# Kernel tuning notes

Hardware: AMD Instinct MI355X
Metric: run time of the kernel (lower is better)

Reference implementation:

```python
import jax, jax.numpy as jnp
import numpy as np

D = 1024
H = 16
B = 4
S = 2048
NEG = -1000000000.0


def setup_inputs() -> dict:
    key = jax.random.key(0)
    ks = jax.random.split(key, 12)
    s = 0.02
    inp = {
        "Q": jax.random.normal(ks[0], (B, S, D), jnp.float32),
        "K": jax.random.normal(ks[1], (B, S, D), jnp.float32),
        "V": jax.random.normal(ks[2], (B, S, D), jnp.float32),
        # causal mask, broadcastable to [B, H, S, S]
        "mask": jnp.broadcast_to(jnp.tril(jnp.ones((S, S), bool)), (B, 1, S, S)),
        "Wq": jax.random.normal(ks[3], (D, D), jnp.float32) * s,
        "bq": jnp.zeros((D,), jnp.float32),
        "Wk": jax.random.normal(ks[4], (D, D), jnp.float32) * s,
        "bk": jnp.zeros((D,), jnp.float32),
        "Wv": jax.random.normal(ks[5], (D, D), jnp.float32) * s,
        "bv": jnp.zeros((D,), jnp.float32),
        "Wo": jax.random.normal(ks[6], (D, D), jnp.float32) * s,
        "bo": jnp.zeros((D,), jnp.float32),
    }
    return inp


def reference(Q, K, V, mask, Wq, bq, Wk, bk, Wv, bv, Wo, bo):
    d = D // H  # head dim
    def split(x):  # [B,S,D] -> [B,H,S,d]
        Bx, Sx, _ = x.shape
        return x.reshape(Bx, Sx, H, d).transpose(0, 2, 1, 3)

    q = split(Q @ Wq + bq)
    k = split(K @ Wk + bk)
    v = split(V @ Wv + bv)

    scores = jnp.einsum("bhsd,bhtd->bhst", q, k) / jnp.sqrt(jnp.float32(d))
    scores = jnp.where(mask, scores, NEG)
    attn = jax.nn.softmax(scores, axis=-1)
    out = jnp.einsum("bhst,bhtd->bhsd", attn, v)  # [B,H,S,d]
    out = out.transpose(0, 2, 1, 3).reshape(Q.shape[0], Q.shape[1], D)
    return out @ Wo + bo
```

## Files before the change

kernel.cpp:

```cpp
#include <hip/hip_runtime.h>
#include <hip/hip_bf16.h>
#include <type_traits>

#define DEV __device__ __forceinline__

typedef short bf16x8 __attribute__((ext_vector_type(8)));
typedef float f32x4 __attribute__((ext_vector_type(4)));
typedef float f32x16 __attribute__((ext_vector_type(16)));
typedef unsigned u32x4 __attribute__((ext_vector_type(4)));

static DEV unsigned short f2bf(float f) {
  unsigned u = __builtin_bit_cast(unsigned, f);
  u += 0x7FFFu + ((u >> 16) & 1u);
  return (unsigned short)(u >> 16);
}

static DEV unsigned cvtpk(float lo, float hi) {
  unsigned d;
  asm("v_cvt_pk_bf16_f32 %0, %1, %2" : "=v"(d) : "v"(lo), "v"(hi));
  return d;
}

static DEV void pl32(unsigned& x, unsigned& y) {
  asm("v_permlane32_swap_b32 %0, %1" : "+v"(x), "+v"(y));
}

static DEV float vmax3(float a, float b, float c) {
  float d;
  asm("v_max3_f32 %0, %1, %2, %3" : "=v"(d) : "v"(a), "v"(b), "v"(c));
  return d;
}

static DEV void gl_lds16(const unsigned short* g, unsigned short* l) {
  __builtin_amdgcn_global_load_lds(
      (const __attribute__((address_space(1))) unsigned*)g,
      (__attribute__((address_space(3))) unsigned*)l, 16, 0, 0);
}

#define QSCALE 0.18033688f

__global__ __launch_bounds__(256) void wtrans4(const float* __restrict__ W0,
                                               const float* __restrict__ W1,
                                               const float* __restrict__ W2,
                                               const float* __restrict__ W3,
                                               unsigned short* __restrict__ T0,
                                               unsigned short* __restrict__ T1,
                                               unsigned short* __restrict__ T2,
                                               unsigned short* __restrict__ T3) {
  const int z = blockIdx.z;
  const float* W = z == 0 ? W0 : z == 1 ? W1 : z == 2 ? W2 : W3;
  unsigned short* Wt = z == 0 ? T0 : z == 1 ? T1 : z == 2 ? T2 : T3;
  const float wsc = (z == 0) ? QSCALE : 1.0f;
  __shared__ __align__(16) unsigned short T[64][72];
  const int tid = threadIdx.x;
  const int k0 = blockIdx.x * 64, n0 = blockIdx.y * 64;
  const int r = tid >> 4, c4 = (tid & 15) * 4;
  for (int j = 0; j < 4; ++j) {
    int row = j * 16 + r;
    float4 v = *(const float4*)&W[(size_t)(k0 + row) * 1024 + n0 + c4];
    ushort4 w;
    w.x = f2bf(v.x * wsc); w.y = f2bf(v.y * wsc);
    w.z = f2bf(v.z * wsc); w.w = f2bf(v.w * wsc);
    *(ushort4*)&T[row][c4] = w;
  }
  __syncthreads();
  for (int j = 0; j < 4; ++j) {
    int n = j * 16 + r;
    ushort4 w;
    w.x = T[c4 + 0][n]; w.y = T[c4 + 1][n]; w.z = T[c4 + 2][n]; w.w = T[c4 + 3][n];
    *(ushort4*)&Wt[(size_t)(n0 + n) * 1024 + k0 + c4] = w;
  }
}

__global__ __launch_bounds__(256) void xcvt3(const float* __restrict__ S0,
                                             const float* __restrict__ S1,
                                             const float* __restrict__ S2,
                                             unsigned short* __restrict__ D0,
                                             unsigned short* __restrict__ D1,
                                             unsigned short* __restrict__ D2) {
  const int z = blockIdx.z;
  const float* S = z == 0 ? S0 : z == 1 ? S1 : S2;
  unsigned short* D = z == 0 ? D0 : z == 1 ? D1 : D2;
  const size_t stride = (size_t)gridDim.x * 256 * 8;
  for (size_t i = ((size_t)blockIdx.x * 256 + threadIdx.x) * 8; i < 8u * 1024 * 1024;
       i += stride) {
    float4 a = *(const float4*)&S[i];
    float4 b = *(const float4*)&S[i + 4];
    uint4 w;
    w.x = cvtpk(a.x, a.y);
    w.y = cvtpk(a.z, a.w);
    w.z = cvtpk(b.x, b.y);
    w.w = cvtpk(b.z, b.w);
    *(uint4*)&D[i] = w;
  }
}

template <typename OutT, bool TRANSV>
DEV void gemm_lds_body(const unsigned short* __restrict__ X,
                       const unsigned short* __restrict__ Wt,
                       const float* __restrict__ bias, OutT* __restrict__ Y,
                       float bsc) {
  __shared__ __align__(16) unsigned short SMG[2 * 128 * 64];
  unsigned short* As = SMG;
  unsigned short* Bs = SMG + 128 * 64;
  const int tid = threadIdx.x, lane = tid & 63, wid = tid >> 6;
  const int m0 = blockIdx.x * 128, n0 = blockIdx.y * 128;
  const int wm = (wid >> 1) * 64, wn = (wid & 1) * 64;
  f32x4 acc[4][4] = {};

  const int srow = wid * 32 + (lane >> 3);
  const int scol = (((lane & 7) ^ ((lane >> 3) & 7))) * 8;
  const unsigned short* gA = &X[(size_t)(m0 + srow) * 1024 + scol];
  const unsigned short* gB = &Wt[(size_t)(n0 + srow) * 1024 + scol];
  unsigned short* lA = &As[wid * 32 * 64];
  unsigned short* lB = &Bs[wid * 32 * 64];

  for (int k0 = 0; k0 < 1024; k0 += 64) {
    __syncthreads();
#pragma unroll
    for (int j = 0; j < 4; ++j) {
      gl_lds16(gA + (size_t)j * 8 * 1024 + k0, lA + j * 8 * 64);
      gl_lds16(gB + (size_t)j * 8 * 1024 + k0, lB + j * 8 * 64);
    }
    __syncthreads();
#pragma unroll
    for (int kk = 0; kk < 2; ++kk) {
      const int kb = ((kk * 4 + (lane >> 4)) ^ (lane & 7)) * 8;
      bf16x8 af[4], bfr[4];
#pragma unroll
      for (int i = 0; i < 4; ++i)
        af[i] = *(const bf16x8*)&As[(wm + i * 16 + (lane & 15)) * 64 + kb];
#pragma unroll
      for (int i = 0; i < 4; ++i)
        bfr[i] = *(const bf16x8*)&Bs[(wn + i * 16 + (lane & 15)) * 64 + kb];
      __builtin_amdgcn_s_setprio(1);
#pragma unroll
      for (int mi = 0; mi < 4; ++mi)
#pragma unroll
        for (int ni = 0; ni < 4; ++ni)
          acc[mi][ni] =
              __builtin_amdgcn_mfma_f32_16x16x32_bf16(af[mi], bfr[ni], acc[mi][ni], 0, 0, 0);
      __builtin_amdgcn_s_setprio(0);
    }
  }

  if constexpr (TRANSV) {
    const int bt = m0 >> 11;
    const int s0 = m0 & 2047;
    const int h0 = n0 >> 6;
    unsigned short* Tl = SMG;
#pragma unroll
    for (int cch = 0; cch < 2; ++cch) {
      __syncthreads();
      if ((wid >> 1) == cch) {
#pragma unroll
        for (int ni = 0; ni < 4; ++ni) {
          const int n = wn + ni * 16 + (lane & 15);
          const float bv = bias[n0 + n] * bsc;
#pragma unroll
          for (int mi = 0; mi < 4; ++mi) {
            const int mloc = mi * 16 + (lane >> 4) * 4;
#pragma unroll
            for (int r = 0; r < 4; r += 2) {
              const unsigned pk = cvtpk(acc[mi][ni][r] + bv, acc[mi][ni][r + 1] + bv);
              *(unsigned*)&Tl[n * 72 + mloc + r] = pk;
            }
          }
        }
      }
      __syncthreads();
      const int m8 = (tid & 7) * 8;
#pragma unroll
      for (int it = 0; it < 4; ++it) {
        const int nr = (tid >> 3) + it * 32;
        const int h = h0 + (nr >> 6), dv = nr & 63;
        uint4 v = *(const uint4*)&Tl[nr * 72 + m8];
        *(uint4*)&((unsigned short*)Y)[(((size_t)bt * 16 + h) * 64 + dv) * 2048 +
                                       s0 + cch * 64 + m8] = v;
      }
    }
  } else {
    for (int ni = 0; ni < 4; ++ni) {
      const int col = n0 + wn + ni * 16 + (lane & 15);
      const float bv = bias[col] * bsc;
      for (int mi = 0; mi < 4; ++mi) {
        const int row = m0 + wm + mi * 16 + (lane >> 4) * 4;
        for (int r = 0; r < 4; ++r) {
          float v = acc[mi][ni][r] + bv;
          if constexpr (std::is_same_v<OutT, float>)
            Y[(size_t)(row + r) * 1024 + col] = v;
          else
            Y[(size_t)(row + r) * 1024 + col] = f2bf(v);
        }
      }
    }
  }
}

__global__ __launch_bounds__(256) void gemm_qkv3(
    const unsigned short* __restrict__ X0, const unsigned short* __restrict__ X1,
    const unsigned short* __restrict__ X2, const unsigned short* __restrict__ W0,
    const unsigned short* __restrict__ W1, const unsigned short* __restrict__ W2,
    const float* __restrict__ b0, const float* __restrict__ b1,
    const float* __restrict__ b2, unsigned short* __restrict__ Y0,
    unsigned short* __restrict__ Y1, unsigned short* __restrict__ Y2, int zoff) {
  const int z = blockIdx.z + zoff;
  const unsigned short* X = z == 0 ? X0 : z == 1 ? X1 : X2;
  const unsigned short* Wt = z == 0 ? W0 : z == 1 ? W1 : W2;
  const float* bias = z == 0 ? b0 : z == 1 ? b1 : b2;
  unsigned short* Y = z == 0 ? Y0 : z == 1 ? Y1 : Y2;
  if (z == 2)
    gemm_lds_body<unsigned short, true>(X, Wt, bias, Y, 1.0f);
  else
    gemm_lds_body<unsigned short, false>(X, Wt, bias, Y, z == 0 ? QSCALE : 1.0f);
}

__global__ __launch_bounds__(256) void gemm_out(const unsigned short* __restrict__ X,
                                                const unsigned short* __restrict__ Wt,
                                                const float* __restrict__ bias,
                                                float* __restrict__ Y) {
  gemm_lds_body<float, false>(X, Wt, bias, Y, 1.0f);
}

__global__ __launch_bounds__(256) void attn_fwd(const unsigned short* __restrict__ Qb,
                                                const unsigned short* __restrict__ Kb,
                                                const unsigned short* __restrict__ Vt,
                                                unsigned short* __restrict__ Ob) {
  constexpr int KP = 72;
  __shared__ __align__(16) unsigned short SM[4 * 64 * KP];
  const int tid = threadIdx.x, lane = tid & 63, wid = tid >> 6;
  const int l31 = lane & 31, hi = lane >> 5;
  const int id = blockIdx.x;
  const int xcd = id & 7, idx = id >> 3;
  const int bh = xcd + 8 * (idx & 7);
  const int qb = idx >> 3;
  const int q0 = (15 - qb) * 128;
  const int b = bh >> 4, h = bh & 15;
  const size_t rowbase = (size_t)b * 2048;
  const int col0 = h * 64;
  const int qmin = q0 + wid * 32;
  const int myq = qmin + l31;
  const unsigned short* Vrow = Vt + (size_t)bh * 64 * 2048;
  const int rr = tid >> 3, c8 = (tid & 7) * 8;

  bf16x8 qf[4];
#pragma unroll
  for (int c = 0; c < 4; ++c)
    qf[c] = *(const bf16x8*)&Qb[(rowbase + myq) * 1024 + col0 + c * 16 + hi * 8];

  const bf16x8 onesv =
      __builtin_bit_cast(bf16x8, (u32x4){0x3F803F80u, 0x3F803F80u, 0x3F803F80u, 0x3F803F80u});

  f32x16 o[2], rsa;
  o[0] = 0.f; o[1] = 0.f; rsa = 0.f;
  float mrow = -1.0e30f;

  const int NT = q0 / 64 + 2;
  uint4 kr0, kr1, vr0, vr1;
#define LOADT(KV0)                                                              \
  do {                                                                          \
    const int _k = (KV0);                                                       \
    kr0 = *(const uint4*)&Kb[(rowbase + _k + rr) * 1024 + col0 + c8];           \
    kr1 = *(const uint4*)&Kb[(rowbase + _k + rr + 32) * 1024 + col0 + c8];      \
    vr0 = *(const uint4*)&Vrow[(size_t)rr * 2048 + _k + c8];                    \
    vr1 = *(const uint4*)&Vrow[(size_t)(rr + 32) * 2048 + _k + c8];             \
  } while (0)

#define WRITET(P)                                                               \
  do {                                                                          \
    unsigned short* Ks_ = SM + (P) * 128 * KP;                                  \
    unsigned short* Vs_ = Ks_ + 64 * KP;                                        \
    *(uint4*)&Ks_[rr * KP + c8] = kr0;                                          \
    *(uint4*)&Ks_[(rr + 32) * KP + c8] = kr1;                                   \
    *(uint4*)&Vs_[rr * KP + c8] = vr0;                                          \
    *(uint4*)&Vs_[(rr + 32) * KP + c8] = vr1;                                   \
  } while (0)

  LOADT(0);
  WRITET(0);
  LOADT(64);
  __syncthreads();

  for (int t = 0; t < NT; ++t) {
    const int kv0 = t * 64;
    const int p = t & 1;
    if (t + 1 < NT) {
      WRITET(p ^ 1);
      if (t + 2 < NT) LOADT(kv0 + 128);
    }
    if (kv0 <= qmin + 31) {
      const unsigned short* Ks = SM + p * 128 * KP;
      const unsigned short* Vs = Ks + 64 * KP;

      f32x16 s2[2];
      s2[0] = 0.f; s2[1] = 0.f;
      __builtin_amdgcn_s_setprio(1);
#pragma unroll
      for (int m = 0; m < 2; ++m)
#pragma unroll
        for (int c = 0; c < 4; ++c) {
          bf16x8 kf = *(const bf16x8*)&Ks[(m * 32 + l31) * KP + c * 16 + hi * 8];
          s2[m] = __builtin_amdgcn_mfma_f32_32x32x16_bf16(kf, qf[c], s2[m], 0, 0, 0);
        }
      __builtin_amdgcn_s_setprio(0);

      if (kv0 + 63 > qmin) {
        const int thr = l31 + (qmin - kv0);
#pragma unroll
        for (int m = 0; m < 2; ++m)
#pragma unroll
          for (int r = 0; r < 16; ++r) {
            const int kvl = m * 32 + (r & 3) + 8 * (r >> 2) + 4 * hi;
            if (kvl > thr) s2[m][r] = -1.0e30f;
          }
      }

      float tmax = fmaxf(s2[0][0], s2[0][1]);
#pragma unroll
      for (int m = 0; m < 2; ++m)
#pragma unroll
        for (int r = m == 0 ? 2 : 0; r < 16; r += 2)
          tmax = vmax3(tmax, s2[m][r], s2[m][r + 1]);
      tmax = fmaxf(tmax, __shfl_xor(tmax, 32));
      if (__any(tmax > mrow + 11.5f)) {
        const float mnew = fmaxf(mrow, tmax);
        const float al = __builtin_amdgcn_exp2f(mrow - mnew);
        mrow = mnew;
        o[0] *= al;
        o[1] *= al;
        rsa[0] *= al;
      }
#pragma unroll
      for (int m = 0; m < 2; ++m)
#pragma unroll
        for (int r = 0; r < 16; ++r)
          s2[m][r] = __builtin_amdgcn_exp2f(s2[m][r] - mrow);

      bf16x8 pf[4];
#pragma unroll
      for (int m = 0; m < 2; ++m) {
        unsigned a0 = cvtpk(s2[m][0], s2[m][1]), a1 = cvtpk(s2[m][2], s2[m][3]);
        unsigned b0 = cvtpk(s2[m][4], s2[m][5]), b1 = cvtpk(s2[m][6], s2[m][7]);
        pl32(a0, b0);
        pl32(a1, b1);
        pf[2 * m] = __builtin_bit_cast(bf16x8, (u32x4){a0, a1, b0, b1});
        unsigned c0 = cvtpk(s2[m][8], s2[m][9]), c1 = cvtpk(s2[m][10], s2[m][11]);
        unsigned d0 = cvtpk(s2[m][12], s2[m][13]), d1 = cvtpk(s2[m][14], s2[m][15]);
        pl32(c0, d0);
        pl32(c1, d1);
        pf[2 * m + 1] = __builtin_bit_cast(bf16x8, (u32x4){c0, c1, d0, d1});
      }

      __builtin_amdgcn_s_setprio(1);
#pragma unroll
      for (int nt = 0; nt < 2; ++nt)
#pragma unroll
        for (int cc = 0; cc < 4; ++cc) {
          bf16x8 vf = *(const bf16x8*)&Vs[(nt * 32 + l31) * KP + cc * 16 + hi * 8];
          o[nt] = __builtin_amdgcn_mfma_f32_32x32x16_bf16(vf, pf[cc], o[nt], 0, 0, 0);
        }
#pragma unroll
      for (int cc = 0; cc < 4; ++cc)
        rsa = __builtin_amdgcn_mfma_f32_32x32x16_bf16(onesv, pf[cc], rsa, 0, 0, 0);
      __builtin_amdgcn_s_setprio(0);
    }
    __syncthreads();
  }
#undef LOADT
#undef WRITET

  unsigned short* Os = SM + wid * 32 * KP;
  const float inv = 1.0f / rsa[0];
#pragma unroll
  for (int nt = 0; nt < 2; ++nt)
#pragma unroll
    for (int rq = 0; rq < 4; ++rq)
#pragma unroll
      for (int j = 0; j < 2; ++j) {
        const int r = rq * 4 + 2 * j;
        const unsigned pk = cvtpk(o[nt][r] * inv, o[nt][r + 1] * inv);
        *(unsigned*)&Os[l31 * KP + nt * 32 + 8 * rq + 4 * hi + 2 * j] = pk;
      }
  __syncthreads();
#pragma unroll
  for (int i = 0; i < 4; ++i) {
    const int qq = (lane >> 3) + i * 8;
    const int dvc = (lane & 7) * 8;
    uint4 val = *(const uint4*)&Os[qq * KP + dvc];
    *(uint4*)&Ob[(rowbase + qmin + qq) * 1024 + col0 + dvc] = val;
  }
}

extern "C" void kernel_launch(void* const* d_in, const int* in_sizes, int n_in,
                              void* d_out, int out_size, void* d_ws, size_t ws_size,
                              hipStream_t stream) {
  const float* Q  = (const float*)d_in[0];
  const float* K  = (const float*)d_in[1];
  const float* V  = (const float*)d_in[2];
  const float* Wq = (const float*)d_in[4];
  const float* bq = (const float*)d_in[5];
  const float* Wk = (const float*)d_in[6];
  const float* bk = (const float*)d_in[7];
  const float* Wv = (const float*)d_in[8];
  const float* bv = (const float*)d_in[9];
  const float* Wo = (const float*)d_in[10];
  const float* bo = (const float*)d_in[11];
  float* out = (float*)d_out;

  const size_t MB = 1024 * 1024;
  char* ws = (char*)d_ws;
  unsigned short* qb  = (unsigned short*)(ws + 0 * MB);
  unsigned short* kb  = (unsigned short*)(ws + 16 * MB);
  unsigned short* vtB = (unsigned short*)(ws + 32 * MB);
  unsigned short* ob  = (unsigned short*)(ws + 48 * MB);
  unsigned short* wtq = (unsigned short*)(ws + 64 * MB);
  unsigned short* wtk = (unsigned short*)(ws + 66 * MB);
  unsigned short* wtv = (unsigned short*)(ws + 68 * MB);
  unsigned short* wto = (unsigned short*)(ws + 70 * MB);

  wtrans4<<<dim3(16, 16, 4), 256, 0, stream>>>(Wq, Wk, Wv, Wo, wtq, wtk, wtv, wto);

  if (ws_size >= 120 * MB) {
    unsigned short* qx = (unsigned short*)(ws + 72 * MB);
    unsigned short* kx = (unsigned short*)(ws + 88 * MB);
    unsigned short* vx = (unsigned short*)(ws + 104 * MB);
    xcvt3<<<dim3(2048, 1, 3), 256, 0, stream>>>(Q, K, V, qx, kx, vx);
    gemm_qkv3<<<dim3(64, 8, 3), 256, 0, stream>>>(qx, kx, vx, wtq, wtk, wtv,
                                                  bq, bk, bv, qb, kb, vtB, 0);
  } else {
    unsigned short* xb = ob;
    const float* Xs[3] = {Q, K, V};
    for (int t = 0; t < 3; ++t) {
      xcvt3<<<dim3(2048, 1, 1), 256, 0, stream>>>(Xs[t], Xs[t], Xs[t], xb, xb, xb);
      gemm_qkv3<<<dim3(64, 8, 1), 256, 0, stream>>>(xb, xb, xb, wtq, wtk, wtv,
                                                    bq, bk, bv, qb, kb, vtB, t);
    }
  }

  attn_fwd<<<1024, 256, 0, stream>>>(qb, kb, vtB, ob);

  gemm_out<<<dim3(64, 8), 256, 0, stream>>>(ob, wto, bo, out);
}
```

Baseline: 187.3 us.

## Split attention into single-wave blocks loading K/V directly from global memory

```diff
diff --git a/kernel.cpp b/kernel.cpp
--- a/kernel.cpp
+++ b/kernel.cpp
@@ -222,26 +222,26 @@
   gemm_lds_body<float, false>(X, Wt, bias, Y, 1.0f);
 }
 
-__global__ __launch_bounds__(256) void attn_fwd(const unsigned short* __restrict__ Qb,
-                                                const unsigned short* __restrict__ Kb,
-                                                const unsigned short* __restrict__ Vt,
-                                                unsigned short* __restrict__ Ob) {
+__global__ __launch_bounds__(64) void attn_fwd(const unsigned short* __restrict__ Qb,
+                                               const unsigned short* __restrict__ Kb,
+                                               const unsigned short* __restrict__ Vt,
+                                               unsigned short* __restrict__ Ob) {
   constexpr int KP = 72;
-  __shared__ __align__(16) unsigned short SM[4 * 64 * KP];
-  const int tid = threadIdx.x, lane = tid & 63, wid = tid >> 6;
+  __shared__ __align__(16) unsigned short Os[32 * KP];
+  const int lane = threadIdx.x;
   const int l31 = lane & 31, hi = lane >> 5;
   const int id = blockIdx.x;
-  const int xcd = id & 7, idx = id >> 3;
-  const int bh = xcd + 8 * (idx & 7);
-  const int qb = idx >> 3;
+  const int bh = (id & 7) + 8 * ((id >> 3) & 7);
+  const int rest = id >> 6;
+  const int qb = rest >> 2;
+  const int sb = rest & 3;
   const int q0 = (15 - qb) * 128;
+  const int qmin = q0 + sb * 32;
+  const int myq = qmin + l31;
   const int b = bh >> 4, h = bh & 15;
   const size_t rowbase = (size_t)b * 2048;
   const int col0 = h * 64;
-  const int qmin = q0 + wid * 32;
-  const int myq = qmin + l31;
   const unsigned short* Vrow = Vt + (size_t)bh * 64 * 2048;
-  const int rr = tid >> 3, c8 = (tid & 7) * 8;
 
   bf16x8 qf[4];
 #pragma unroll
@@ -255,121 +255,92 @@
   o[0] = 0.f; o[1] = 0.f; rsa = 0.f;
   float mrow = -1.0e30f;
 
-  const int NT = q0 / 64 + 2;
-  uint4 kr0, kr1, vr0, vr1;
-#define LOADT(KV0)                                                              \
-  do {                                                                          \
-    const int _k = (KV0);                                                       \
-    kr0 = *(const uint4*)&Kb[(rowbase + _k + rr) * 1024 + col0 + c8];           \
-    kr1 = *(const uint4*)&Kb[(rowbase + _k + rr + 32) * 1024 + col0 + c8];      \
-    vr0 = *(const uint4*)&Vrow[(size_t)rr * 2048 + _k + c8];                    \
-    vr1 = *(const uint4*)&Vrow[(size_t)(rr + 32) * 2048 + _k + c8];             \
-  } while (0)
-
-#define WRITET(P)                                                               \
-  do {                                                                          \
-    unsigned short* Ks_ = SM + (P) * 128 * KP;                                  \
-    unsigned short* Vs_ = Ks_ + 64 * KP;                                        \
-    *(uint4*)&Ks_[rr * KP + c8] = kr0;                                          \
-    *(uint4*)&Ks_[(rr + 32) * KP + c8] = kr1;                                   \
-    *(uint4*)&Vs_[rr * KP + c8] = vr0;                                          \
-    *(uint4*)&Vs_[(rr + 32) * KP + c8] = vr1;                                   \
-  } while (0)
-
-  LOADT(0);
-  WRITET(0);
-  LOADT(64);
-  __syncthreads();
-
-  for (int t = 0; t < NT; ++t) {
+  const int NTw = qmin / 64 + 1;
+  for (int t = 0; t < NTw; ++t) {
     const int kv0 = t * 64;
-    const int p = t & 1;
-    if (t + 1 < NT) {
-      WRITET(p ^ 1);
-      if (t + 2 < NT) LOADT(kv0 + 128);
-    }
-    if (kv0 <= qmin + 31) {
-      const unsigned short* Ks = SM + p * 128 * KP;
-      const unsigned short* Vs = Ks + 64 * KP;
-
-      f32x16 s2[2];
-      s2[0] = 0.f; s2[1] = 0.f;
-      __builtin_amdgcn_s_setprio(1);
+    bf16x8 kf[2][4], vf[2][4];
+#pragma unroll
+    for (int m = 0; m < 2; ++m)
+#pragma unroll
+      for (int c = 0; c < 4; ++c)
+        kf[m][c] = *(const bf16x8*)&Kb[(rowbase + kv0 + m * 32 + l31) * 1024 +
+                                       col0 + c * 16 + hi * 8];
+#pragma unroll
+    for (int nt = 0; nt < 2; ++nt)
+#pragma unroll
+      for (int cc = 0; cc < 4; ++cc)
+        vf[nt][cc] = *(const bf16x8*)&Vrow[(size_t)(nt * 32 + l31) * 2048 +
+                                           kv0 + cc * 16 + hi * 8];
+
+    f32x16 s2[2];
+    s2[0] = 0.f; s2[1] = 0.f;
+    __builtin_amdgcn_s_setprio(1);
+#pragma unroll
+    for (int m = 0; m < 2; ++m)
+#pragma unroll
+      for (int c = 0; c < 4; ++c)
+        s2[m] = __builtin_amdgcn_mfma_f32_32x32x16_bf16(kf[m][c], qf[c], s2[m], 0, 0, 0);
+    __builtin_amdgcn_s_setprio(0);
+
+    if (kv0 + 63 > qmin) {
+      const int thr = l31 + (qmin - kv0);
 #pragma unroll
       for (int m = 0; m < 2; ++m)
 #pragma unroll
-        for (int c = 0; c < 4; ++c) {
-          bf16x8 kf = *(const bf16x8*)&Ks[(m * 32 + l31) * KP + c * 16 + hi * 8];
-          s2[m] = __builtin_amdgcn_mfma_f32_32x32x16_bf16(kf, qf[c], s2[m], 0, 0, 0);
+        for (int r = 0; r < 16; ++r) {
+          const int kvl = m * 32 + (r & 3) + 8 * (r >> 2) + 4 * hi;
+          if (kvl > thr) s2[m][r] = -1.0e30f;
         }
-      __builtin_amdgcn_s_setprio(0);
-
-      if (kv0 + 63 > qmin) {
-        const int thr = l31 + (qmin - kv0);
-#pragma unroll
-        for (int m = 0; m < 2; ++m)
-#pragma unroll
-          for (int r = 0; r < 16; ++r) {
-            const int kvl = m * 32 + (r & 3) + 8 * (r >> 2) + 4 * hi;
-            if (kvl > thr) s2[m][r] = -1.0e30f;
-          }
-      }
-
-      float tmax = fmaxf(s2[0][0], s2[0][1]);
-#pragma unroll
-      for (int m = 0; m < 2; ++m)
-#pragma unroll
-        for (int r = m == 0 ? 2 : 0; r < 16; r += 2)
-          tmax = vmax3(tmax, s2[m][r], s2[m][r + 1]);
-      tmax = fmaxf(tmax, __shfl_xor(tmax, 32));
-      if (__any(tmax > mrow + 11.5f)) {
-        const float mnew = fmaxf(mrow, tmax);
-        const float al = __builtin_amdgcn_exp2f(mrow - mnew);
-        mrow = mnew;
-        o[0] *= al;
-        o[1] *= al;
-        rsa[0] *= al;
-      }
-#pragma unroll
-      for (int m = 0; m < 2; ++m)
-#pragma unroll
-        for (int r = 0; r < 16; ++r)
-          s2[m][r] = __builtin_amdgcn_exp2f(s2[m][r] - mrow);
-
-      bf16x8 pf[4];
-#pragma unroll
-      for (int m = 0; m < 2; ++m) {
-        unsigned a0 = cvtpk(s2[m][0], s2[m][1]), a1 = cvtpk(s2[m][2], s2[m][3]);
-        unsigned b0 = cvtpk(s2[m][4], s2[m][5]), b1 = cvtpk(s2[m][6], s2[m][7]);
-        pl32(a0, b0);
-        pl32(a1, b1);
-        pf[2 * m] = __builtin_bit_cast(bf16x8, (u32x4){a0, a1, b0, b1});
-        unsigned c0 = cvtpk(s2[m][8], s2[m][9]), c1 = cvtpk(s2[m][10], s2[m][11]);
-        unsigned d0 = cvtpk(s2[m][12], s2[m][13]), d1 = cvtpk(s2[m][14], s2[m][15]);
-        pl32(c0, d0);
-        pl32(c1, d1);
-        pf[2 * m + 1] = __builtin_bit_cast(bf16x8, (u32x4){c0, c1, d0, d1});
-      }
-
-      __builtin_amdgcn_s_setprio(1);
-#pragma unroll
-      for (int nt = 0; nt < 2; ++nt)
-#pragma unroll
-        for (int cc = 0; cc < 4; ++cc) {
-          bf16x8 vf = *(const bf16x8*)&Vs[(nt * 32 + l31) * KP + cc * 16 + hi * 8];
-          o[nt] = __builtin_amdgcn_mfma_f32_32x32x16_bf16(vf, pf[cc], o[nt], 0, 0, 0);
-        }
+    }
+
+    float tmax = fmaxf(s2[0][0], s2[0][1]);
+#pragma unroll
+    for (int m = 0; m < 2; ++m)
+#pragma unroll
+      for (int r = m == 0 ? 2 : 0; r < 16; r += 2)
+        tmax = vmax3(tmax, s2[m][r], s2[m][r + 1]);
+    tmax = fmaxf(tmax, __shfl_xor(tmax, 32));
+    if (__any(tmax > mrow + 11.5f)) {
+      const float mnew = fmaxf(mrow, tmax);
+      const float al = __builtin_amdgcn_exp2f(mrow - mnew);
+      mrow = mnew;
+      o[0] *= al;
+      o[1] *= al;
+      rsa[0] *= al;
+    }
+#pragma unroll
+    for (int m = 0; m < 2; ++m)
+#pragma unroll
+      for (int r = 0; r < 16; ++r)
+        s2[m][r] = __builtin_amdgcn_exp2f(s2[m][r] - mrow);
+
+    bf16x8 pf[4];
+#pragma unroll
+    for (int m = 0; m < 2; ++m) {
+      unsigned a0 = cvtpk(s2[m][0], s2[m][1]), a1 = cvtpk(s2[m][2], s2[m][3]);
+      unsigned b0 = cvtpk(s2[m][4], s2[m][5]), b1 = cvtpk(s2[m][6], s2[m][7]);
+      pl32(a0, b0);
+      pl32(a1, b1);
+      pf[2 * m] = __builtin_bit_cast(bf16x8, (u32x4){a0, a1, b0, b1});
+      unsigned c0 = cvtpk(s2[m][8], s2[m][9]), c1 = cvtpk(s2[m][10], s2[m][11]);
+      unsigned d0 = cvtpk(s2[m][12], s2[m][13]), d1 = cvtpk(s2[m][14], s2[m][15]);
+      pl32(c0, d0);
+      pl32(c1, d1);
+      pf[2 * m + 1] = __builtin_bit_cast(bf16x8, (u32x4){c0, c1, d0, d1});
+    }
+
+    __builtin_amdgcn_s_setprio(1);
+#pragma unroll
+    for (int nt = 0; nt < 2; ++nt)
 #pragma unroll
       for (int cc = 0; cc < 4; ++cc)
-        rsa = __builtin_amdgcn_mfma_f32_32x32x16_bf16(onesv, pf[cc], rsa, 0, 0, 0);
-      __builtin_amdgcn_s_setprio(0);
-    }
-    __syncthreads();
-  }
-#undef LOADT
-#undef WRITET
-
-  unsigned short* Os = SM + wid * 32 * KP;
+        o[nt] = __builtin_amdgcn_mfma_f32_32x32x16_bf16(vf[nt][cc], pf[cc], o[nt], 0, 0, 0);
+#pragma unroll
+    for (int cc = 0; cc < 4; ++cc)
+      rsa = __builtin_amdgcn_mfma_f32_32x32x16_bf16(onesv, pf[cc], rsa, 0, 0, 0);
+    __builtin_amdgcn_s_setprio(0);
+  }
+
   const float inv = 1.0f / rsa[0];
 #pragma unroll
   for (int nt = 0; nt < 2; ++nt)
@@ -437,7 +408,7 @@
     }
   }
 
-  attn_fwd<<<1024, 256, 0, stream>>>(qb, kb, vtB, ob);
+  attn_fwd<<<4096, 64, 0, stream>>>(qb, kb, vtB, ob);
 
   gemm_out<<<dim3(64, 8), 256, 0, stream>>>(ob, wto, bo, out);
 }
```

Result: slower. 246.4 us (+31.5%).
